# Kernel optimization log

Measured on AMD Instinct MI355X. Metric: run time of the kernel, lower is better.

Reference implementation:

```python
import jax, jax.numpy as jnp
import numpy as np

B, H, D = 1, 24, 128
TXT, REDUX, IMG, REF, ROUTER, NC = 512, 64, 2048, 512, 32, 2
S = TXT + REDUX + IMG + REF + ROUTER
REF_SHIFT = 1.5  # model_config['ref_shift'] (nonzero to exercise the mask path)


def setup_inputs() -> dict:
    rng = jax.random.key(0)
    k1, k2, k3, k4, k5 = jax.random.split(rng, 5)
    tri = TXT + REDUX + IMG
    return {
        "query": jax.random.normal(k1, (B, H, S, D), jnp.float32),
        "key": jax.random.normal(k2, (B, H, S, D), jnp.float32),
        "value": jax.random.normal(k3, (B, H, S, D), jnp.float32),
        "ref_mask": jax.random.uniform(k4, (B, REF, tri), jnp.float32),
        "routing_map": jax.random.uniform(k5, (B, NC, IMG), jnp.float32),
        "txt_seq_len": TXT,
        "redux_seq_len": REDUX,
        "img_seq_len": IMG,
        "ref_seq_len": REF,
        "router_seq_len": ROUTER,
        "num_conds": NC,
    }


def _sdpa(q, k, v, mask=None):
    # torch F.scaled_dot_product_attention semantics (additive mask)
    scale = 1.0 / jnp.sqrt(jnp.asarray(q.shape[-1], q.dtype))
    logits = jnp.einsum('...qd,...kd->...qk', q, k) * scale
    if mask is not None:
        logits = logits + mask  # mask broadcasts over heads
    return jnp.einsum('...qk,...kd->...qd', jax.nn.softmax(logits, axis=-1), v)


def reference(query, key, value, ref_mask, routing_map,
              txt_seq_len, redux_seq_len, img_seq_len, ref_seq_len,
              router_seq_len, num_conds):
    b = query.shape[0]
    te = txt_seq_len                 # text end
    tre = te + redux_seq_len         # text+redux end
    tri = tre + img_seq_len          # text+redux+image end
    trir = tri + ref_seq_len         # +ref end

    # ---- additive attention mask (only the used [:tri, :trir] slice; broadcast over heads)
    mask = jnp.zeros((b, 1, tri, trir), query.dtype)
    mask = mask.at[:, :, :tri, tri:trir].add(REF_SHIFT)
    # ref_mask: [B, ref, tri] -> transpose -> [B, 1, tri, ref], (m-1)*100
    rm = (jnp.swapaxes(ref_mask, -1, -2)[:, None] - 1.0) * 100.0
    mask = mask.at[:, :, :tri, tri:trir].add(rm)
    # routing map for redux keys: [B, nc, img] -> repeat per-cond -> [B, redux, img] -> [B,1,img,redux]
    rep = redux_seq_len // num_conds
    redux_rt = (jnp.repeat(routing_map, rep, axis=1) - 1.0) * 100.0
    mask = mask.at[:, :, tre:tri, te:tre].add(jnp.swapaxes(redux_rt, 1, 2)[:, None])
    # routing map for ref keys: [B, nc, img] -> [B, ref, img] -> [B,1,img,ref]
    rep = ref_seq_len // num_conds
    ref_rt = (jnp.repeat(routing_map, rep, axis=1) - 1.0) * 100.0
    mask = mask.at[:, :, tre:tri, tri:trir].add(jnp.swapaxes(ref_rt, 1, 2)[:, None])

    # ---- segment 1: text+redux+image queries attend to text+redux+image+ref keys
    out1 = _sdpa(query[:, :, :tri], key[:, :, :trir], value[:, :, :trir], mask)

    # ---- segment 2: per-condition ref self-attention (block-diagonal over num_conds)
    h = query.shape[1]
    rq = query[:, :, tri:trir].reshape(b, h, num_conds, -1, D)
    rk = key[:, :, tri:trir].reshape(b, h, num_conds, -1, D)
    rv = value[:, :, tri:trir].reshape(b, h, num_conds, -1, D)
    ref_out = _sdpa(rq, rk, rv).reshape(b, h, ref_seq_len, D)

    # ---- segment 3: router queries attend to [image keys ; router keys]
    qr = query[:, :, trir:]
    kr = jnp.concatenate([key[:, :, tre:tri], key[:, :, trir:]], axis=2)
    vr = jnp.concatenate([value[:, :, tre:tri], value[:, :, trir:]], axis=2)
    router_out = _sdpa(qr, kr, vr)

    return jnp.concatenate([out1, ref_out, router_out], axis=2)
```

## Files before the change

kernel.cpp:

```cpp
#include <hip/hip_runtime.h>
#include <hip/hip_bf16.h>

#define TXT   512
#define REDUX 64
#define IMG   2048
#define REFN  512
#define NC    2
#define SEQ   3168
#define DH    128
#define NH    24
#define TRE   576
#define TRI   2624
#define TRIR  3136
#define SCALE 0.08838834764831845f
#define L2E   1.4426950408889634f
#define QSC   (SCALE * L2E)
#define C100  (100.0f * L2E)
#define CREF  (98.5f * L2E)
#define THR2  (4.0f * L2E)

using f32x4  = __attribute__((ext_vector_type(4))) float;
using short8 = __attribute__((ext_vector_type(8))) short;

__device__ inline short f2bf(float x) {
    union { __hip_bfloat16 b; short s; } u;
    u.b = __float2bfloat16(x);
    return u.s;
}

__device__ inline void gload16(const short* g, short* l) {
    __builtin_amdgcn_global_load_lds(
        (const __attribute__((address_space(1))) unsigned int*)g,
        (__attribute__((address_space(3))) unsigned int*)l, 16, 0, 0);
}

__global__ void cvt_kv_kernel(const float* __restrict__ K, const float* __restrict__ V,
                              short* __restrict__ Kb, short* __restrict__ Vt) {
    const int h   = blockIdx.y;
    const int tid = threadIdx.x;
    {
        const int base = ((h * SEQ + blockIdx.x * 16) * DH) >> 2;
        #pragma unroll
        for (int j = 0; j < 2; ++j) {
            const int i = base + tid + j * 256;
            const float4 v = ((const float4*)K)[i];
            short4 o;
            o.x = f2bf(v.x); o.y = f2bf(v.y); o.z = f2bf(v.z); o.w = f2bf(v.w);
            ((short4*)Kb)[i] = o;
        }
    }
    {
        const int s8 = blockIdx.x * 2 + (tid >> 7);
        const int d  = tid & 127;
        const int s0 = s8 * 8;
        const float* src = V + ((size_t)h * SEQ + s0) * DH + d;
        short8 w;
        #pragma unroll
        for (int j = 0; j < 8; ++j) w[j] = f2bf(src[j * DH]);
        const int tb   = s0 & ~63;
        const int j0   = s0 & 63;
        const int ks2  = j0 >> 5;
        const int jm   = j0 & 15;
        const int hi   = (j0 >> 4) & 1;
        const int pos0 = ks2 * 32 + (jm >> 2) * 8 + hi * 4;
        short* dst = Vt + ((size_t)h * DH + d) * SEQ + tb;
        short4 lo4, hi4;
        lo4.x = w[0]; lo4.y = w[1]; lo4.z = w[2]; lo4.w = w[3];
        hi4.x = w[4]; hi4.y = w[5]; hi4.z = w[6]; hi4.w = w[7];
        *(short4*)(dst + pos0)     = lo4;
        *(short4*)(dst + pos0 + 8) = hi4;
    }
}

__global__ __launch_bounds__(256, 2)
void attn_mfma(const float* __restrict__ Q, const short* __restrict__ Kb,
               const short* __restrict__ Vtg, const float* __restrict__ ref_mask,
               const float* __restrict__ routing, float* __restrict__ out)
{
    __shared__ short Ks[64 * 128];
    __shared__ short Vs[128 * 64];

    const int bid  = blockIdx.x;
    const int h    = bid % NH;
    const int bx   = bid / NH;
    const int tid  = threadIdx.x;
    const int wave = tid >> 6, lane = tid & 63;
    const int g    = lane >> 4, l4 = lane & 15;

    int qbase, ks0 = 0, ntiles;
    bool masked = false, router = false;
    if (bx < 21)       { qbase = bx * 128; ntiles = 49; masked = true; }
    else if (bx == 21) { qbase = TRIR; ntiles = 33; router = true; }
    else {
        const int b2 = bx - 22;
        qbase = TRI + b2 * 128;
        ks0 = TRI + (b2 >> 1) * 256; ntiles = 4;
    }

    const int rbase = qbase + wave * 32;
    const bool valid = !(masked && rbase >= TRI) && !(router && wave >= 1);

    const short* KbH = Kb  + (size_t)h * SEQ * DH;
    const short* VtH = Vtg + (size_t)h * DH * SEQ;
    int koff[4], vD[4], vKC[4], voff[4];
    short *ksd[4], *vsd[4];
    #pragma unroll
    for (int j = 0; j < 4; ++j) {
        const int ci = tid + j * 256;
        const int kk = ci >> 4, kc = ci & 15;
        koff[j] = kk * 128 + ((kc ^ (kk & 7)) << 3);
        const int vd = ci >> 3, vk = ci & 7;
        vD[j] = vd; vKC[j] = vk;
        voff[j] = vd * SEQ + ((vk ^ (vd & 7)) << 3);
        ksd[j] = Ks + (size_t)(j * 256 + wave * 64) * 8;
        vsd[j] = Vs + (size_t)(j * 256 + wave * 64) * 8;
    }

    short8 qA[2][4];
    if (valid) {
        #pragma unroll
        for (int qt = 0; qt < 2; ++qt) {
            const int q = rbase + qt * 16 + l4;
            const float* qp = Q + ((size_t)h * SEQ + q) * DH;
            #pragma unroll
            for (int ks = 0; ks < 4; ++ks) {
                const float4 a = *(const float4*)(qp + ks * 32 + g * 8);
                const float4 b = *(const float4*)(qp + ks * 32 + g * 8 + 4);
                short8 f;
                f[0] = f2bf(a.x * QSC); f[1] = f2bf(a.y * QSC);
                f[2] = f2bf(a.z * QSC); f[3] = f2bf(a.w * QSC);
                f[4] = f2bf(b.x * QSC); f[5] = f2bf(b.y * QSC);
                f[6] = f2bf(b.z * QSC); f[7] = f2bf(b.w * QSC);
                qA[qt][ks] = f;
            }
        }
    }

    f32x4 acc[2][8] = {};
    float m_run[2] = {-3.0e38f, -3.0e38f}, l_run[2] = {0.f, 0.f};
    const int bsrc = (lane >> 4) << 2;

    for (int t = 0; t < ntiles; ++t) {
        const int kt = masked ? t * 64
                     : (router ? (t < 32 ? TRE + t * 64 : TRIR) : ks0 + t * 64);
        const bool tail = router && (t == 32);
        __syncthreads();
        const short* kb = KbH + (size_t)kt * DH;
        const short* vb = VtH + kt;
        #pragma unroll
        for (int j = 0; j < 4; ++j) {
            const int ko = tail ? (koff[j] & 4095) : koff[j];
            gload16(kb + ko, ksd[j]);
        }
        #pragma unroll
        for (int j = 0; j < 4; ++j) {
            const int vo = tail ? (vD[j] * SEQ + (((vKC[j] ^ (vD[j] & 7)) & 3) << 3))
                                : voff[j];
            gload16(vb + vo, vsd[j]);
        }
        __syncthreads();

        if (!valid) continue;

        f32x4 s[2][4] = {};
        __builtin_amdgcn_s_setprio(1);
        #pragma unroll
        for (int nt = 0; nt < 4; ++nt) {
            const int key = nt * 16 + l4;
            #pragma unroll
            for (int ks = 0; ks < 4; ++ks) {
                const short8 kB = *(const short8*)(Ks + key * 128 + (((ks * 4 + g) ^ (key & 7)) << 3));
                s[0][nt] = __builtin_amdgcn_mfma_f32_16x16x32_bf16(kB, qA[0][ks], s[0][nt], 0, 0, 0);
                s[1][nt] = __builtin_amdgcn_mfma_f32_16x16x32_bf16(kB, qA[1][ks], s[1][nt], 0, 0, 0);
            }
        }
        __builtin_amdgcn_s_setprio(0);

        if (masked) {
            if (kt >= TRI) {
                const int cr = (kt - TRI) >> 8;
                const int j0 = kt - TRI + g * 4;
                #pragma unroll
                for (int qt = 0; qt < 2; ++qt) {
                    const int q  = rbase + qt * 16 + l4;
                    const bool hr = rbase >= TRE;
                    float radd = 0.f;
                    if (hr) radd = routing[cr * IMG + (q - TRE)] * C100 - C100;
                    #pragma unroll
                    for (int nt = 0; nt < 4; ++nt)
                        #pragma unroll
                        for (int r = 0; r < 4; ++r) {
                            const float rmv = ref_mask[(size_t)(j0 + nt * 16 + r) * TRI + q];
                            s[qt][nt][r] += rmv * C100 - CREF + radd;
                        }
                }
            } else if (kt == TXT) {
                if (rbase >= TRE) {
                    #pragma unroll
                    for (int qt = 0; qt < 2; ++qt) {
                        const int q = rbase + qt * 16 + l4;
                        const float a0 = routing[q - TRE] * C100 - C100;
                        const float a1 = routing[IMG + q - TRE] * C100 - C100;
                        #pragma unroll
                        for (int nt = 0; nt < 4; ++nt)
                            #pragma unroll
                            for (int r = 0; r < 4; ++r)
                                s[qt][nt][r] += (nt >> 1) ? a1 : a0;
                    }
                }
            }
        }
        if (tail) {
            #pragma unroll
            for (int qt = 0; qt < 2; ++qt)
                #pragma unroll
                for (int r = 0; r < 4; ++r) { s[qt][2][r] = -3.0e38f; s[qt][3][r] = -3.0e38f; }
        }

        float mx[2];
        #pragma unroll
        for (int qt = 0; qt < 2; ++qt) {
            float m0 = fmaxf(fmaxf(s[qt][0][0], s[qt][0][1]), fmaxf(s[qt][0][2], s[qt][0][3]));
            m0 = fmaxf(m0, fmaxf(fmaxf(s[qt][1][0], s[qt][1][1]), fmaxf(s[qt][1][2], s[qt][1][3])));
            m0 = fmaxf(m0, fmaxf(fmaxf(s[qt][2][0], s[qt][2][1]), fmaxf(s[qt][2][2], s[qt][2][3])));
            m0 = fmaxf(m0, fmaxf(fmaxf(s[qt][3][0], s[qt][3][1]), fmaxf(s[qt][3][2], s[qt][3][3])));
            m0 = fmaxf(m0, __shfl_xor(m0, 16));
            m0 = fmaxf(m0, __shfl_xor(m0, 32));
            mx[qt] = m0;
        }

        const float gmax = fmaxf(mx[0] - m_run[0], mx[1] - m_run[1]);
        if (__any(gmax > THR2)) {
            #pragma unroll
            for (int qt = 0; qt < 2; ++qt) {
                const float mn    = fmaxf(m_run[qt], mx[qt]);
                const float corrq = exp2f(m_run[qt] - mn);
                m_run[qt] = mn;
                l_run[qt] *= corrq;
                f32x4 corr;
                #pragma unroll
                for (int r = 0; r < 4; ++r) corr[r] = __shfl(corrq, bsrc + r);
                #pragma unroll
                for (int nt = 0; nt < 8; ++nt)
                    #pragma unroll
                    for (int r = 0; r < 4; ++r) acc[qt][nt][r] *= corr[r];
            }
        }

        short8 pA[2][2];
        #pragma unroll
        for (int qt = 0; qt < 2; ++qt) {
            float rsum = 0.f;
            #pragma unroll
            for (int nt = 0; nt < 4; ++nt)
                #pragma unroll
                for (int r = 0; r < 4; ++r) {
                    s[qt][nt][r] = exp2f(s[qt][nt][r] - m_run[qt]);
                    rsum += s[qt][nt][r];
                }
            rsum += __shfl_xor(rsum, 16);
            rsum += __shfl_xor(rsum, 32);
            l_run[qt] += rsum;
            #pragma unroll
            for (int j = 0; j < 4; ++j) {
                pA[qt][0][j]     = f2bf(s[qt][0][j]);
                pA[qt][0][4 + j] = f2bf(s[qt][1][j]);
                pA[qt][1][j]     = f2bf(s[qt][2][j]);
                pA[qt][1][4 + j] = f2bf(s[qt][3][j]);
            }
        }

        __builtin_amdgcn_s_setprio(1);
        #pragma unroll
        for (int ks2 = 0; ks2 < 2; ++ks2) {
            const int kc = ks2 * 4 + g;
            #pragma unroll
            for (int nt = 0; nt < 8; ++nt) {
                const int d = nt * 16 + l4;
                const short8 vB = *(const short8*)(Vs + d * 64 + ((kc ^ (d & 7)) << 3));
                acc[0][nt] = __builtin_amdgcn_mfma_f32_16x16x32_bf16(pA[0][ks2], vB, acc[0][nt], 0, 0, 0);
                acc[1][nt] = __builtin_amdgcn_mfma_f32_16x16x32_bf16(pA[1][ks2], vB, acc[1][nt], 0, 0, 0);
            }
        }
        __builtin_amdgcn_s_setprio(0);
    }

    if (valid) {
        #pragma unroll
        for (int qt = 0; qt < 2; ++qt) {
            f32x4 linv;
            #pragma unroll
            for (int r = 0; r < 4; ++r) linv[r] = 1.0f / __shfl(l_run[qt], bsrc + r);
            #pragma unroll
            for (int nt = 0; nt < 8; ++nt)
                #pragma unroll
                for (int r = 0; r < 4; ++r) {
                    const int q = rbase + qt * 16 + g * 4 + r;
                    out[((size_t)h * SEQ + q) * DH + nt * 16 + l4] = acc[qt][nt][r] * linv[r];
                }
        }
    }
}

#define KT  32
#define LDK (DH + 4)
__global__ __launch_bounds__(256, 2)
void anystory_attn_scalar(const float* __restrict__ Q, const float* __restrict__ K,
                          const float* __restrict__ V, const float* __restrict__ ref_mask,
                          const float* __restrict__ routing, float* __restrict__ out, int row0)
{
    __shared__ float KsS[KT][LDK];
    __shared__ float VsS[KT][LDK];

    const int h    = blockIdx.y;
    const int r0   = row0 + blockIdx.x * 4;
    const int tid  = threadIdx.x;
    const int wave = tid >> 6;
    const int lane = tid & 63;
    const int key_l = lane & 31;
    const int half  = lane >> 5;
    const int row  = r0 + wave;

    int rs0, re0, rs1 = 0, re1 = 0;
    bool masked = false;
    if (r0 < TRI) { rs0 = 0; re0 = TRIR; masked = true; }
    else if (r0 < TRIR) {
        int c = (r0 - TRI) / (REFN / NC);
        rs0 = TRI + c * (REFN / NC); re0 = rs0 + (REFN / NC);
    } else { rs0 = TRE; re0 = TRI; rs1 = TRIR; re1 = SEQ; }

    float4 qreg[16];
    const float4* qptr = (const float4*)(Q + ((size_t)h * SEQ + row) * DH + half * 64);
    #pragma unroll
    for (int i = 0; i < 16; ++i) qreg[i] = qptr[i];

    float m = -1e30f, l = 0.f, acc0 = 0.f, acc1 = 0.f;

    for (int range = 0; range < 2; ++range) {
        const int ks = (range == 0) ? rs0 : rs1;
        const int ke = (range == 0) ? re0 : re1;
        for (int kt = ks; kt < ke; kt += KT) {
            __syncthreads();
            #pragma unroll
            for (int i = 0; i < 4; ++i) {
                int idx = tid + i * 256;
                int rr = idx >> 5, cc = (idx & 31) * 4;
                const float4 kv = ((const float4*)(K + ((size_t)h * SEQ + kt + rr) * DH))[idx & 31];
                const float4 vv = ((const float4*)(V + ((size_t)h * SEQ + kt + rr) * DH))[idx & 31];
                *(float4*)&KsS[rr][cc] = kv;
                *(float4*)&VsS[rr][cc] = vv;
            }
            __syncthreads();

            const int kglob = kt + key_l;
            float dot = 0.f;
            #pragma unroll
            for (int i = 0; i < 16; ++i) {
                float4 k4 = *(const float4*)&KsS[key_l][half * 64 + i * 4];
                dot += qreg[i].x * k4.x + qreg[i].y * k4.y + qreg[i].z * k4.z + qreg[i].w * k4.w;
            }
            dot += __shfl_xor(dot, 32);
            float logit = dot * SCALE;

            if (masked) {
                if (kglob >= TRI) {
                    logit += 1.5f + (ref_mask[(size_t)(kglob - TRI) * TRI + row] - 1.f) * 100.f;
                    if (row >= TRE)
                        logit += (routing[((kglob - TRI) >> 8) * IMG + (row - TRE)] - 1.f) * 100.f;
                } else if (kglob >= TXT && kglob < TRE && row >= TRE) {
                    logit += (routing[((kglob - TXT) >> 5) * IMG + (row - TRE)] - 1.f) * 100.f;
                }
            }

            float tm = logit;
            tm = fmaxf(tm, __shfl_xor(tm, 1));
            tm = fmaxf(tm, __shfl_xor(tm, 2));
            tm = fmaxf(tm, __shfl_xor(tm, 4));
            tm = fmaxf(tm, __shfl_xor(tm, 8));
            tm = fmaxf(tm, __shfl_xor(tm, 16));
            const float nm   = fmaxf(m, tm);
            const float corr = __expf(m - nm);
            const float p    = __expf(logit - nm);
            float ps = p;
            ps += __shfl_xor(ps, 1);
            ps += __shfl_xor(ps, 2);
            ps += __shfl_xor(ps, 4);
            ps += __shfl_xor(ps, 8);
            ps += __shfl_xor(ps, 16);
            l = l * corr + ps;
            acc0 *= corr; acc1 *= corr;
            m = nm;

            #pragma unroll
            for (int k = 0; k < KT; ++k) {
                const float pk = __shfl(p, k);
                acc0 += pk * VsS[k][lane];
                acc1 += pk * VsS[k][lane + 64];
            }
        }
    }

    const float inv = 1.f / l;
    float* op = out + ((size_t)h * SEQ + row) * DH;
    op[lane]      = acc0 * inv;
    op[lane + 64] = acc1 * inv;
}

extern "C" void kernel_launch(void* const* d_in, const int* in_sizes, int n_in,
                              void* d_out, int out_size, void* d_ws, size_t ws_size,
                              hipStream_t stream) {
    const float* Q        = (const float*)d_in[0];
    const float* K        = (const float*)d_in[1];
    const float* V        = (const float*)d_in[2];
    const float* ref_mask = (const float*)d_in[3];
    const float* routing  = (const float*)d_in[4];
    float* out = (float*)d_out;

    const size_t elems = (size_t)NH * SEQ * DH;
    const size_t need  = 2 * elems * sizeof(short);

    if (ws_size < need) {
        dim3 grid(SEQ / 4, NH);
        anystory_attn_scalar<<<grid, 256, 0, stream>>>(Q, K, V, ref_mask, routing, out, 0);
        return;
    }

    short* Kb  = (short*)d_ws;
    short* Vtg = Kb + elems;

    cvt_kv_kernel<<<dim3(SEQ / 16, NH), 256, 0, stream>>>(K, V, Kb, Vtg);

    attn_mfma<<<dim3(NH * 26), 256, 0, stream>>>(Q, Kb, Vtg, ref_mask, routing, out);
}
```

Measured before the change: 237.3 us.

## Split each key tile across two wave groups and merge softmax partials in LDS

Measured after the change: 311.2 us. 31.1% more time.

```diff
diff --git a/kernel.cpp b/kernel.cpp
--- a/kernel.cpp
+++ b/kernel.cpp
@@ -72,13 +72,16 @@
     }
 }
 
-__global__ __launch_bounds__(256, 2)
+__global__ __launch_bounds__(512, 2)
 void attn_mfma(const float* __restrict__ Q, const short* __restrict__ Kb,
                const short* __restrict__ Vtg, const float* __restrict__ ref_mask,
                const float* __restrict__ routing, float* __restrict__ out)
 {
-    __shared__ short Ks[64 * 128];
-    __shared__ short Vs[128 * 64];
+    __shared__ short smem[33280];
+    short* Ks = smem;
+    short* Vs = smem + 8192;
+    float* accA = (float*)smem;
+    float* mlA  = (float*)(smem + 32768);
 
     const int bid  = blockIdx.x;
     const int h    = bid % NH;
@@ -86,6 +89,8 @@
     const int tid  = threadIdx.x;
     const int wave = tid >> 6, lane = tid & 63;
     const int g    = lane >> 4, l4 = lane & 15;
+    const int qg   = wave & 3;
+    const int kh   = wave >> 2;
 
     int qbase, ks0 = 0, ntiles;
     bool masked = false, router = false;
@@ -97,24 +102,25 @@
         ks0 = TRI + (b2 >> 1) * 256; ntiles = 4;
     }
 
-    const int rbase = qbase + wave * 32;
-    const bool valid = !(masked && rbase >= TRI) && !(router && wave >= 1);
+    const int rbase = qbase + qg * 32;
+    const bool valid = !(masked && rbase >= TRI) && !(router && qg >= 1);
 
     const short* KbH = Kb  + (size_t)h * SEQ * DH;
     const short* VtH = Vtg + (size_t)h * DH * SEQ;
-    int koff[4], vD[4], vKC[4], voff[4];
-    short *ksd[4], *vsd[4];
+    int koff[2], vD[2], vKC[2], voff[2];
     #pragma unroll
-    for (int j = 0; j < 4; ++j) {
-        const int ci = tid + j * 256;
+    for (int j = 0; j < 2; ++j) {
+        const int ci = tid + j * 512;
         const int kk = ci >> 4, kc = ci & 15;
         koff[j] = kk * 128 + ((kc ^ (kk & 7)) << 3);
         const int vd = ci >> 3, vk = ci & 7;
         vD[j] = vd; vKC[j] = vk;
         voff[j] = vd * SEQ + ((vk ^ (vd & 7)) << 3);
-        ksd[j] = Ks + (size_t)(j * 256 + wave * 64) * 8;
-        vsd[j] = Vs + (size_t)(j * 256 + wave * 64) * 8;
-    }
+    }
+    short* ksd0 = Ks + (size_t)(wave * 64) * 8;
+    short* ksd1 = Ks + (size_t)(512 + wave * 64) * 8;
+    short* vsd0 = Vs + (size_t)(wave * 64) * 8;
+    short* vsd1 = Vs + (size_t)(512 + wave * 64) * 8;
 
     short8 qA[2][4];
     if (valid) {
@@ -147,26 +153,25 @@
         __syncthreads();
         const short* kb = KbH + (size_t)kt * DH;
         const short* vb = VtH + kt;
-        #pragma unroll
-        for (int j = 0; j < 4; ++j) {
-            const int ko = tail ? (koff[j] & 4095) : koff[j];
-            gload16(kb + ko, ksd[j]);
-        }
-        #pragma unroll
-        for (int j = 0; j < 4; ++j) {
-            const int vo = tail ? (vD[j] * SEQ + (((vKC[j] ^ (vD[j] & 7)) & 3) << 3))
-                                : voff[j];
-            gload16(vb + vo, vsd[j]);
+        {
+            const int ko0 = tail ? (koff[0] & 4095) : koff[0];
+            const int ko1 = tail ? (koff[1] & 4095) : koff[1];
+            gload16(kb + ko0, ksd0);
+            gload16(kb + ko1, ksd1);
+            const int vo0 = tail ? (vD[0] * SEQ + (((vKC[0] ^ (vD[0] & 7)) & 3) << 3)) : voff[0];
+            const int vo1 = tail ? (vD[1] * SEQ + (((vKC[1] ^ (vD[1] & 7)) & 3) << 3)) : voff[1];
+            gload16(vb + vo0, vsd0);
+            gload16(vb + vo1, vsd1);
         }
         __syncthreads();
 
         if (!valid) continue;
 
-        f32x4 s[2][4] = {};
+        f32x4 s[2][2] = {};
         __builtin_amdgcn_s_setprio(1);
         #pragma unroll
-        for (int nt = 0; nt < 4; ++nt) {
-            const int key = nt * 16 + l4;
+        for (int nt = 0; nt < 2; ++nt) {
+            const int key = kh * 32 + nt * 16 + l4;
             #pragma unroll
             for (int ks = 0; ks < 4; ++ks) {
                 const short8 kB = *(const short8*)(Ks + key * 128 + (((ks * 4 + g) ^ (key & 7)) << 3));
@@ -179,7 +184,7 @@
         if (masked) {
             if (kt >= TRI) {
                 const int cr = (kt - TRI) >> 8;
-                const int j0 = kt - TRI + g * 4;
+                const int j0 = kt - TRI + kh * 32 + g * 4;
                 #pragma unroll
                 for (int qt = 0; qt < 2; ++qt) {
                     const int q  = rbase + qt * 16 + l4;
@@ -187,7 +192,7 @@
                     float radd = 0.f;
                     if (hr) radd = routing[cr * IMG + (q - TRE)] * C100 - C100;
                     #pragma unroll
-                    for (int nt = 0; nt < 4; ++nt)
+                    for (int nt = 0; nt < 2; ++nt)
                         #pragma unroll
                         for (int r = 0; r < 4; ++r) {
                             const float rmv = ref_mask[(size_t)(j0 + nt * 16 + r) * TRI + q];
@@ -199,22 +204,23 @@
                     #pragma unroll
                     for (int qt = 0; qt < 2; ++qt) {
                         const int q = rbase + qt * 16 + l4;
-                        const float a0 = routing[q - TRE] * C100 - C100;
-                        const float a1 = routing[IMG + q - TRE] * C100 - C100;
+                        const float a = routing[kh * IMG + q - TRE] * C100 - C100;
                         #pragma unroll
-                        for (int nt = 0; nt < 4; ++nt)
+                        for (int nt = 0; nt < 2; ++nt)
                             #pragma unroll
                             for (int r = 0; r < 4; ++r)
-                                s[qt][nt][r] += (nt >> 1) ? a1 : a0;
+                                s[qt][nt][r] += a;
                     }
                 }
             }
         }
-        if (tail) {
+        if (tail && kh) {
             #pragma unroll
             for (int qt = 0; qt < 2; ++qt)
                 #pragma unroll
-                for (int r = 0; r < 4; ++r) { s[qt][2][r] = -3.0e38f; s[qt][3][r] = -3.0e38f; }
+                for (int nt = 0; nt < 2; ++nt)
+                    #pragma unroll
+                    for (int r = 0; r < 4; ++r) s[qt][nt][r] = -3.0e38f;
         }
 
         float mx[2];
@@ -222,8 +228,6 @@
         for (int qt = 0; qt < 2; ++qt) {
             float m0 = fmaxf(fmaxf(s[qt][0][0], s[qt][0][1]), fmaxf(s[qt][0][2], s[qt][0][3]));
             m0 = fmaxf(m0, fmaxf(fmaxf(s[qt][1][0], s[qt][1][1]), fmaxf(s[qt][1][2], s[qt][1][3])));
-            m0 = fmaxf(m0, fmaxf(fmaxf(s[qt][2][0], s[qt][2][1]), fmaxf(s[qt][2][2], s[qt][2][3])));
-            m0 = fmaxf(m0, fmaxf(fmaxf(s[qt][3][0], s[qt][3][1]), fmaxf(s[qt][3][2], s[qt][3][3])));
             m0 = fmaxf(m0, __shfl_xor(m0, 16));
             m0 = fmaxf(m0, __shfl_xor(m0, 32));
             mx[qt] = m0;
@@ -247,12 +251,12 @@
             }
         }
 
-        short8 pA[2][2];
+        short8 pA[2];
         #pragma unroll
         for (int qt = 0; qt < 2; ++qt) {
             float rsum = 0.f;
             #pragma unroll
-            for (int nt = 0; nt < 4; ++nt)
+            for (int nt = 0; nt < 2; ++nt)
                 #pragma unroll
                 for (int r = 0; r < 4; ++r) {
                     s[qt][nt][r] = exp2f(s[qt][nt][r] - m_run[qt]);
@@ -263,41 +267,69 @@
             l_run[qt] += rsum;
             #pragma unroll
             for (int j = 0; j < 4; ++j) {
-                pA[qt][0][j]     = f2bf(s[qt][0][j]);
-                pA[qt][0][4 + j] = f2bf(s[qt][1][j]);
-                pA[qt][1][j]     = f2bf(s[qt][2][j]);
-                pA[qt][1][4 + j] = f2bf(s[qt][3][j]);
+                pA[qt][j]     = f2bf(s[qt][0][j]);
+                pA[qt][4 + j] = f2bf(s[qt][1][j]);
             }
         }
 
         __builtin_amdgcn_s_setprio(1);
-        #pragma unroll
-        for (int ks2 = 0; ks2 < 2; ++ks2) {
-            const int kc = ks2 * 4 + g;
+        {
+            const int kc = kh * 4 + g;
             #pragma unroll
             for (int nt = 0; nt < 8; ++nt) {
                 const int d = nt * 16 + l4;
                 const short8 vB = *(const short8*)(Vs + d * 64 + ((kc ^ (d & 7)) << 3));
-                acc[0][nt] = __builtin_amdgcn_mfma_f32_16x16x32_bf16(pA[0][ks2], vB, acc[0][nt], 0, 0, 0);
-                acc[1][nt] = __builtin_amdgcn_mfma_f32_16x16x32_bf16(pA[1][ks2], vB, acc[1][nt], 0, 0, 0);
+                acc[0][nt] = __builtin_amdgcn_mfma_f32_16x16x32_bf16(pA[0], vB, acc[0][nt], 0, 0, 0);
+                acc[1][nt] = __builtin_amdgcn_mfma_f32_16x16x32_bf16(pA[1], vB, acc[1][nt], 0, 0, 0);
             }
         }
         __builtin_amdgcn_s_setprio(0);
     }
 
-    if (valid) {
+    __syncthreads();
+    if (valid && kh == 1) {
+        float* ab = accA + qg * 4096;
+        #pragma unroll
+        for (int qt = 0; qt < 2; ++qt)
+            #pragma unroll
+            for (int nt = 0; nt < 8; ++nt)
+                *(f32x4*)(ab + ((qt * 8 + nt) * 64 + lane) * 4) = acc[qt][nt];
+        if (g == 0) {
+            #pragma unroll
+            for (int qt = 0; qt < 2; ++qt) {
+                mlA[qg * 32 + qt * 16 + l4]       = m_run[qt];
+                mlA[128 + qg * 32 + qt * 16 + l4] = l_run[qt];
+            }
+        }
+    }
+    __syncthreads();
+    if (valid && kh == 0) {
+        const float* ab = accA + qg * 4096;
         #pragma unroll
         for (int qt = 0; qt < 2; ++qt) {
-            f32x4 linv;
-            #pragma unroll
-            for (int r = 0; r < 4; ++r) linv[r] = 1.0f / __shfl(l_run[qt], bsrc + r);
-            #pragma unroll
-            for (int nt = 0; nt < 8; ++nt)
+            const float m1 = mlA[qg * 32 + qt * 16 + l4];
+            const float l1 = mlA[128 + qg * 32 + qt * 16 + l4];
+            const float mm = fmaxf(m_run[qt], m1);
+            const float w0 = exp2f(m_run[qt] - mm);
+            const float w1 = exp2f(m1 - mm);
+            const float inv = 1.0f / (l_run[qt] * w0 + l1 * w1);
+            const float ow0 = w0 * inv, ow1 = w1 * inv;
+            f32x4 v0, v1;
+            #pragma unroll
+            for (int r = 0; r < 4; ++r) {
+                v0[r] = __shfl(ow0, bsrc + r);
+                v1[r] = __shfl(ow1, bsrc + r);
+            }
+            #pragma unroll
+            for (int nt = 0; nt < 8; ++nt) {
+                const f32x4 aL = *(const f32x4*)(ab + ((qt * 8 + nt) * 64 + lane) * 4);
                 #pragma unroll
                 for (int r = 0; r < 4; ++r) {
                     const int q = rbase + qt * 16 + g * 4 + r;
-                    out[((size_t)h * SEQ + q) * DH + nt * 16 + l4] = acc[qt][nt][r] * linv[r];
+                    out[((size_t)h * SEQ + q) * DH + nt * 16 + l4] =
+                        acc[qt][nt][r] * v0[r] + aL[r] * v1[r];
                 }
+            }
         }
     }
 }
@@ -430,5 +462,5 @@
 
     cvt_kv_kernel<<<dim3(SEQ / 16, NH), 256, 0, stream>>>(K, V, Kb, Vtg);
 
-    attn_mfma<<<dim3(NH * 26), 256, 0, stream>>>(Q, Kb, Vtg, ref_mask, routing, out);
-}
+    attn_mfma<<<dim3(NH * 26), 512, 0, stream>>>(Q, Kb, Vtg, ref_mask, routing, out);
+}
```
